# Kernel optimization log

Hardware: AMD Instinct MI355X
Metric: run time of the kernel (lower is better)

Reference implementation:

```python
import jax, jax.numpy as jnp
import numpy as np

N, E = 50000, 800000
IN_DIM, E_DIM, OUT_DIM, H = 128, 32, 16, 4
NEG_SLOPE = 0.2


def setup_inputs() -> dict:
    key = jax.random.key(0)
    ks = jax.random.split(key, 9)
    return {
        "feat": jax.random.normal(ks[0], (N, IN_DIM), jnp.float32),
        "edge_attr": jax.random.normal(ks[1], (E, E_DIM), jnp.float32),
        "src": jax.random.randint(ks[2], (E,), 0, N),
        "dst": jax.random.randint(ks[3], (E,), 0, N),
        "W_fc": jax.random.normal(ks[4], (OUT_DIM * H, IN_DIM), jnp.float32) * 0.1,
        "W_edge": jax.random.normal(ks[5], (OUT_DIM * H, E_DIM), jnp.float32) * 0.1,
        "attn_h": jax.random.normal(ks[6], (1, H, OUT_DIM), jnp.float32) * 0.1,
        "attn_t": jax.random.normal(ks[7], (1, H, OUT_DIM), jnp.float32) * 0.1,
        "attn_e": jax.random.normal(ks[8], (1, H, OUT_DIM), jnp.float32) * 0.1,
        "bias": jnp.zeros((1, H, OUT_DIM), jnp.float32),
    }


def reference(feat, edge_attr, src, dst, W_fc, W_edge, attn_h, attn_t, attn_e, bias):
    n = feat.shape[0]
    # node / edge projections
    feat_ = (feat @ W_fc.T).reshape(n, H, OUT_DIM)          # [N,H,D]
    eh = (feat_ * attn_h).sum(-1)                            # [N,H]
    et = (feat_ * attn_t).sum(-1)                            # [N,H]
    feat_e = (edge_attr @ W_edge.T).reshape(-1, H, OUT_DIM)  # [E,H,D]
    ee = (feat_e * attn_e).sum(-1)                           # [E,H]
    # per-edge attention logits: u_add_e then e_add_v, then leaky relu
    e = eh[src] + ee + et[dst]                               # [E,H]
    e = jnp.where(e > 0, e, NEG_SLOPE * e)
    # edge softmax grouped by destination node
    e_max = jax.ops.segment_max(e, dst, num_segments=n)      # [N,H]
    e_max = jnp.where(jnp.isfinite(e_max), e_max, 0.0)
    a = jnp.exp(e - e_max[dst])                              # [E,H]
    a_sum = jax.ops.segment_sum(a, dst, num_segments=n)      # [N,H]
    a = a / jnp.where(a_sum[dst] > 0, a_sum[dst], 1.0)
    # u_mul_e + sum aggregation
    msg = feat_[src] * a[:, :, None]                         # [E,H,D]
    rst = jax.ops.segment_sum(msg, dst, num_segments=n)      # [N,H,D]
    rst = rst + bias
    return rst.reshape(n, H * OUT_DIM)                       # concat_out
```

## Files before the change

kernel.cpp:

```cpp
#include <hip/hip_runtime.h>

#define NN 50000
#define EE 800000
#define IND 128
#define EDD 32
#define ODD 16
#define NH 4
#define HD 64
#define NEG_SLOPE 0.2f
#define NBLK ((NN + 255) / 256)

__global__ __launch_bounds__(256)
void k_init(int* __restrict__ deg) {
    int i = blockIdx.x * 256 + threadIdx.x;
    if (i < NN) deg[i] = 0;
}

__global__ __launch_bounds__(256)
void k_prep(const float* __restrict__ W_fc, const float* __restrict__ W_edge,
            const float* __restrict__ attn_e,
            float* __restrict__ Wt, float* __restrict__ w_ee) {
    int i = blockIdx.x * 256 + threadIdx.x;
    if (i < HD * IND) {
        int k = i >> 6, j = i & 63;
        Wt[i] = W_fc[j * IND + k];
    }
    if (i < NH * EDD) {
        int h = i >> 5, k = i & 31;
        float s = 0.f;
        for (int d = 0; d < ODD; ++d)
            s += W_edge[(h * ODD + d) * EDD + k] * attn_e[h * ODD + d];
        w_ee[i] = s;
    }
}

__global__ __launch_bounds__(256)
void k_node(const float* __restrict__ feat, const float* __restrict__ Wt,
            const float* __restrict__ attn_h, const float* __restrict__ attn_t,
            float* __restrict__ feat_ws, float2* __restrict__ eh2,
            float2* __restrict__ et2) {
    int n = blockIdx.x * 256 + threadIdx.x;
    int half = blockIdx.y;
    if (n >= NN) return;
    const int jbase = half * 32;
    float4 row[32];
    const float4* fr4 = (const float4*)(feat + (long)n * IND);
#pragma unroll
    for (int q = 0; q < 32; ++q) row[q] = fr4[q];
    asm volatile("" ::: "memory");
    float acc[32];
#pragma unroll
    for (int j = 0; j < 32; ++j) acc[j] = 0.f;
#pragma unroll
    for (int k0 = 0; k0 < 32; ++k0) {
        float f[4] = {row[k0].x, row[k0].y, row[k0].z, row[k0].w};
#pragma unroll
        for (int kk = 0; kk < 4; ++kk) {
            const float* w = Wt + (k0 * 4 + kk) * HD + jbase;
#pragma unroll
            for (int j = 0; j < 32; ++j) acc[j] += f[kk] * w[j];
        }
    }
    float4* d4 = (float4*)(feat_ws + (long)n * HD + jbase);
#pragma unroll
    for (int q = 0; q < 8; ++q)
        d4[q] = make_float4(acc[q*4], acc[q*4+1], acc[q*4+2], acc[q*4+3]);
    float sh[2], st[2];
#pragma unroll
    for (int hh = 0; hh < 2; ++hh) {
        sh[hh] = 0.f; st[hh] = 0.f;
        int hg = half * 2 + hh;
#pragma unroll
        for (int d = 0; d < ODD; ++d) {
            float av = acc[hh * ODD + d];
            sh[hh] += av * attn_h[hg * ODD + d];
            st[hh] += av * attn_t[hg * ODD + d];
        }
    }
    eh2[n * 2 + half] = make_float2(sh[0], sh[1]);
    et2[n * 2 + half] = make_float2(st[0], st[1]);
}

__global__ __launch_bounds__(256)
void k_hist(const int* __restrict__ dst, int* __restrict__ deg, int* __restrict__ rank) {
    int e = blockIdx.x * 256 + threadIdx.x;
    if (e < EE) rank[e] = atomicAdd(&deg[dst[e]], 1);
}

__global__ __launch_bounds__(256)
void k_scan1(const int* __restrict__ deg, int* __restrict__ offs, int* __restrict__ part) {
    __shared__ int s[256];
    int t = threadIdx.x, i = blockIdx.x * 256 + t;
    int v = (i < NN) ? deg[i] : 0;
    s[t] = v;
    __syncthreads();
#pragma unroll
    for (int o = 1; o < 256; o <<= 1) {
        int u = (t >= o) ? s[t - o] : 0;
        __syncthreads();
        if (t >= o) s[t] += u;
        __syncthreads();
    }
    if (i < NN) offs[i] = s[t] - v;
    if (t == 255) part[blockIdx.x] = s[255];
}

__global__ __launch_bounds__(256)
void k_scan2(int* __restrict__ part) {
    __shared__ int s[256];
    int t = threadIdx.x;
    int v = (t < NBLK) ? part[t] : 0;
    s[t] = v;
    __syncthreads();
#pragma unroll
    for (int o = 1; o < 256; o <<= 1) {
        int u = (t >= o) ? s[t - o] : 0;
        __syncthreads();
        if (t >= o) s[t] += u;
        __syncthreads();
    }
    if (t < NBLK) part[t] = s[t] - v;
}

__global__ __launch_bounds__(256)
void k_scan3(int* __restrict__ offs, const int* __restrict__ part) {
    int i = blockIdx.x * 256 + threadIdx.x;
    if (i < NN) offs[i] += part[i >> 8];
}

__global__ __launch_bounds__(256)
void k_logit(const float* __restrict__ edge_attr, const int* __restrict__ src,
             const int* __restrict__ dst, const float* __restrict__ w_ee,
             const float4* __restrict__ eh4, const float4* __restrict__ et4,
             const int* __restrict__ offs, const int* __restrict__ rank,
             float4* __restrict__ e_buf4, int* __restrict__ perm) {
    int t = blockIdx.x * 256 + threadIdx.x;
    int e0 = t * 2;
    if (e0 >= EE) return;
    int2 s2 = *(const int2*)(src + e0);
    int2 d2 = *(const int2*)(dst + e0);
    int2 r2 = *(const int2*)(rank + e0);
    int   o0 = offs[d2.x], o1 = offs[d2.y];
    float4 vh0 = eh4[s2.x], vh1 = eh4[s2.y];
    float4 vt0 = et4[d2.x], vt1 = et4[d2.y];
    const float4* ea = (const float4*)(edge_attr + (long)e0 * EDD);
    float4 r[16];
#pragma unroll
    for (int c = 0; c < 16; ++c) r[c] = ea[c];
    asm volatile("" ::: "memory");
    const float* f0 = (const float*)&r[0];
    const float* f1 = (const float*)&r[8];
    float x0[NH], x1[NH];
#pragma unroll
    for (int h = 0; h < NH; ++h) {
        float a = 0.f, b = 0.f;
#pragma unroll
        for (int k = 0; k < EDD; ++k) {
            float w = w_ee[h * EDD + k];
            a += f0[k] * w;
            b += f1[k] * w;
        }
        x0[h] = a; x1[h] = b;
    }
    x0[0] += vh0.x + vt0.x; x0[1] += vh0.y + vt0.y;
    x0[2] += vh0.z + vt0.z; x0[3] += vh0.w + vt0.w;
    x1[0] += vh1.x + vt1.x; x1[1] += vh1.y + vt1.y;
    x1[2] += vh1.z + vt1.z; x1[3] += vh1.w + vt1.w;
#pragma unroll
    for (int h = 0; h < NH; ++h) {
        float v0 = x0[h], v1 = x1[h];
        v0 = v0 > 0.f ? v0 : NEG_SLOPE * v0;
        v1 = v1 > 0.f ? v1 : NEG_SLOPE * v1;
        x0[h] = __expf(v0);
        x1[h] = __expf(v1);
    }
    e_buf4[e0]     = make_float4(x0[0], x0[1], x0[2], x0[3]);
    e_buf4[e0 + 1] = make_float4(x1[0], x1[1], x1[2], x1[3]);
    perm[o0 + r2.x] = e0;
    perm[o1 + r2.y] = e0 + 1;
}

__global__ __launch_bounds__(256)
void k_reduce(const int* __restrict__ offs, const int* __restrict__ deg,
              const float* __restrict__ e_buf, const int* __restrict__ perm,
              const int* __restrict__ src, const float* __restrict__ feat_ws,
              const float* __restrict__ bias, float* __restrict__ out) {
    int wid = (blockIdx.x * 256 + threadIdx.x) >> 6;
    int lane = threadIdx.x & 63;
    if (wid >= NN) return;
    int start = __builtin_amdgcn_readfirstlane(offs[wid]);
    int dn    = __builtin_amdgcn_readfirstlane(deg[wid]);
    int h = lane >> 4;
    int q = lane & 15;
    float acc = 0.f, l = 0.f;

    for (int c0 = 0; c0 < dn; c0 += 16) {
        int rem = dn - c0; if (rem > 16) rem = 16;
        int qq = (q < rem) ? q : (rem - 1);
        int   e_q = perm[start + c0 + qq];
        int   s_q = src[e_q];
        float a_q = (q < rem) ? e_buf[(long)e_q * 4 + h] : 0.f;
        float f[16];
#pragma unroll
        for (int i = 0; i < 16; ++i) {
            int si = __shfl(s_q, i);
            f[i] = feat_ws[(long)si * HD + lane];
        }
#pragma unroll
        for (int i = 0; i < 16; ++i) {
            float ai = __shfl(a_q, (lane & 48) + i);
            l += ai;
            acc += ai * f[i];
        }
    }
    float res = (l > 0.f) ? acc / l : 0.f;
    out[(long)wid * HD + lane] = res + bias[lane];
}

extern "C" void kernel_launch(void* const* d_in, const int* in_sizes, int n_in,
                              void* d_out, int out_size, void* d_ws, size_t ws_size,
                              hipStream_t stream) {
    const float* feat      = (const float*)d_in[0];
    const float* edge_attr = (const float*)d_in[1];
    const int*   src       = (const int*)d_in[2];
    const int*   dst       = (const int*)d_in[3];
    const float* W_fc      = (const float*)d_in[4];
    const float* W_edge    = (const float*)d_in[5];
    const float* attn_h    = (const float*)d_in[6];
    const float* attn_t    = (const float*)d_in[7];
    const float* attn_e    = (const float*)d_in[8];
    const float* bias      = (const float*)d_in[9];
    float* out             = (float*)d_out;

    float* ws        = (float*)d_ws;
    float4* e_buf4   = (float4*)ws;
    float4* eh4      = e_buf4 + EE;
    float4* et4      = eh4 + NN;
    float*  feat_ws  = (float*)(et4 + NN);
    float*  Wt       = feat_ws + (long)NN * HD;
    float*  w_ee     = Wt + HD * IND;
    int*    perm     = (int*)(w_ee + NH * EDD);
    int*    rank     = perm + EE;
    int*    deg      = rank + EE;
    int*    offs     = deg + NN;
    int*    part     = offs + NN;

    k_init<<<NBLK, 256, 0, stream>>>(deg);
    k_prep<<<(HD * IND + 255) / 256, 256, 0, stream>>>(W_fc, W_edge, attn_e, Wt, w_ee);
    dim3 ngrid(NBLK, 2);
    k_node<<<ngrid, 256, 0, stream>>>(feat, Wt, attn_h, attn_t, feat_ws,
                                      (float2*)eh4, (float2*)et4);
    k_hist<<<(EE + 255) / 256, 256, 0, stream>>>(dst, deg, rank);
    k_scan1<<<NBLK, 256, 0, stream>>>(deg, offs, part);
    k_scan2<<<1, 256, 0, stream>>>(part);
    k_scan3<<<NBLK, 256, 0, stream>>>(offs, part);
    k_logit<<<(EE / 2 + 255) / 256, 256, 0, stream>>>(edge_attr, src, dst, w_ee, eh4, et4,
                                                      offs, rank, e_buf4, perm);
    k_reduce<<<(NN * 64 + 255) / 256, 256, 0, stream>>>(offs, deg, (const float*)e_buf4,
                                                        perm, src, feat_ws, bias, out);
}
```

Baseline: 340.7 us.

## Move logit assembly and exp into reduce kernel; merge init and prep

The per-edge logit kernel now stores only the edge-attribute projection. The gather of eh[src] and et[dst], the leaky-relu and the exp move into the per-destination reduce kernel, which already has src per edge and et for its own node. This drops the src and eh/et gathers from the logit pass and merges two tiny setup kernels into one launch. In exchange the reduce kernel adds a random eh gather per edge and the exp work.

```diff
diff --git a/kernel.cpp b/kernel.cpp
--- a/kernel.cpp
+++ b/kernel.cpp
@@ -11,16 +11,11 @@
 #define NBLK ((NN + 255) / 256)
 
 __global__ __launch_bounds__(256)
-void k_init(int* __restrict__ deg) {
+void k_init_prep(int* __restrict__ deg, const float* __restrict__ W_fc,
+                 const float* __restrict__ W_edge, const float* __restrict__ attn_e,
+                 float* __restrict__ Wt, float* __restrict__ w_ee) {
     int i = blockIdx.x * 256 + threadIdx.x;
     if (i < NN) deg[i] = 0;
-}
-
-__global__ __launch_bounds__(256)
-void k_prep(const float* __restrict__ W_fc, const float* __restrict__ W_edge,
-            const float* __restrict__ attn_e,
-            float* __restrict__ Wt, float* __restrict__ w_ee) {
-    int i = blockIdx.x * 256 + threadIdx.x;
     if (i < HD * IND) {
         int k = i >> 6, j = i & 63;
         Wt[i] = W_fc[j * IND + k];
@@ -129,20 +124,16 @@
 }
 
 __global__ __launch_bounds__(256)
-void k_logit(const float* __restrict__ edge_attr, const int* __restrict__ src,
-             const int* __restrict__ dst, const float* __restrict__ w_ee,
-             const float4* __restrict__ eh4, const float4* __restrict__ et4,
-             const int* __restrict__ offs, const int* __restrict__ rank,
-             float4* __restrict__ e_buf4, int* __restrict__ perm) {
+void k_logit2(const float* __restrict__ edge_attr, const int* __restrict__ dst,
+              const float* __restrict__ w_ee, const int* __restrict__ offs,
+              const int* __restrict__ rank, float4* __restrict__ ee4,
+              int* __restrict__ perm) {
     int t = blockIdx.x * 256 + threadIdx.x;
     int e0 = t * 2;
     if (e0 >= EE) return;
-    int2 s2 = *(const int2*)(src + e0);
     int2 d2 = *(const int2*)(dst + e0);
     int2 r2 = *(const int2*)(rank + e0);
     int   o0 = offs[d2.x], o1 = offs[d2.y];
-    float4 vh0 = eh4[s2.x], vh1 = eh4[s2.y];
-    float4 vt0 = et4[d2.x], vt1 = et4[d2.y];
     const float4* ea = (const float4*)(edge_attr + (long)e0 * EDD);
     float4 r[16];
 #pragma unroll
@@ -162,27 +153,16 @@
         }
         x0[h] = a; x1[h] = b;
     }
-    x0[0] += vh0.x + vt0.x; x0[1] += vh0.y + vt0.y;
-    x0[2] += vh0.z + vt0.z; x0[3] += vh0.w + vt0.w;
-    x1[0] += vh1.x + vt1.x; x1[1] += vh1.y + vt1.y;
-    x1[2] += vh1.z + vt1.z; x1[3] += vh1.w + vt1.w;
-#pragma unroll
-    for (int h = 0; h < NH; ++h) {
-        float v0 = x0[h], v1 = x1[h];
-        v0 = v0 > 0.f ? v0 : NEG_SLOPE * v0;
-        v1 = v1 > 0.f ? v1 : NEG_SLOPE * v1;
-        x0[h] = __expf(v0);
-        x1[h] = __expf(v1);
-    }
-    e_buf4[e0]     = make_float4(x0[0], x0[1], x0[2], x0[3]);
-    e_buf4[e0 + 1] = make_float4(x1[0], x1[1], x1[2], x1[3]);
+    ee4[e0]     = make_float4(x0[0], x0[1], x0[2], x0[3]);
+    ee4[e0 + 1] = make_float4(x1[0], x1[1], x1[2], x1[3]);
     perm[o0 + r2.x] = e0;
     perm[o1 + r2.y] = e0 + 1;
 }
 
 __global__ __launch_bounds__(256)
 void k_reduce(const int* __restrict__ offs, const int* __restrict__ deg,
-              const float* __restrict__ e_buf, const int* __restrict__ perm,
+              const float* __restrict__ ee, const float* __restrict__ eh,
+              const float* __restrict__ et, const int* __restrict__ perm,
               const int* __restrict__ src, const float* __restrict__ feat_ws,
               const float* __restrict__ bias, float* __restrict__ out) {
     int wid = (blockIdx.x * 256 + threadIdx.x) >> 6;
@@ -192,6 +172,7 @@
     int dn    = __builtin_amdgcn_readfirstlane(deg[wid]);
     int h = lane >> 4;
     int q = lane & 15;
+    float et_h = et[(long)wid * 4 + h];
     float acc = 0.f, l = 0.f;
 
     for (int c0 = 0; c0 < dn; c0 += 16) {
@@ -199,7 +180,11 @@
         int qq = (q < rem) ? q : (rem - 1);
         int   e_q = perm[start + c0 + qq];
         int   s_q = src[e_q];
-        float a_q = (q < rem) ? e_buf[(long)e_q * 4 + h] : 0.f;
+        float ee_q = ee[(long)e_q * 4 + h];
+        float eh_q = eh[(long)s_q * 4 + h];
+        float x = ee_q + eh_q + et_h;
+        x = x > 0.f ? x : NEG_SLOPE * x;
+        float a_q = (q < rem) ? __expf(x) : 0.f;
         float f[16];
 #pragma unroll
         for (int i = 0; i < 16; ++i) {
@@ -233,8 +218,8 @@
     float* out             = (float*)d_out;
 
     float* ws        = (float*)d_ws;
-    float4* e_buf4   = (float4*)ws;
-    float4* eh4      = e_buf4 + EE;
+    float4* ee4      = (float4*)ws;
+    float4* eh4      = ee4 + EE;
     float4* et4      = eh4 + NN;
     float*  feat_ws  = (float*)(et4 + NN);
     float*  Wt       = feat_ws + (long)NN * HD;
@@ -245,8 +230,7 @@
     int*    offs     = deg + NN;
     int*    part     = offs + NN;
 
-    k_init<<<NBLK, 256, 0, stream>>>(deg);
-    k_prep<<<(HD * IND + 255) / 256, 256, 0, stream>>>(W_fc, W_edge, attn_e, Wt, w_ee);
+    k_init_prep<<<NBLK, 256, 0, stream>>>(deg, W_fc, W_edge, attn_e, Wt, w_ee);
     dim3 ngrid(NBLK, 2);
     k_node<<<ngrid, 256, 0, stream>>>(feat, Wt, attn_h, attn_t, feat_ws,
                                       (float2*)eh4, (float2*)et4);
@@ -254,8 +238,9 @@
     k_scan1<<<NBLK, 256, 0, stream>>>(deg, offs, part);
     k_scan2<<<1, 256, 0, stream>>>(part);
     k_scan3<<<NBLK, 256, 0, stream>>>(offs, part);
-    k_logit<<<(EE / 2 + 255) / 256, 256, 0, stream>>>(edge_attr, src, dst, w_ee, eh4, et4,
-                                                      offs, rank, e_buf4, perm);
-    k_reduce<<<(NN * 64 + 255) / 256, 256, 0, stream>>>(offs, deg, (const float*)e_buf4,
+    k_logit2<<<(EE / 2 + 255) / 256, 256, 0, stream>>>(edge_attr, dst, w_ee, offs, rank,
+                                                       ee4, perm);
+    k_reduce<<<(NN * 64 + 255) / 256, 256, 0, stream>>>(offs, deg, (const float*)ee4,
+                                                        (const float*)eh4, (const float*)et4,
                                                         perm, src, feat_ws, bias, out);
 }
```

After: 334.6 us. Within noise of the previous version (-1.8%).
